# Optimization experiments

Measured on AMD Instinct MI355X. Metric: run time of the kernel, lower is better.

Reference implementation:

```python
import jax, jax.numpy as jnp
import numpy as np

C = 256
EPS = 1e-5
SHIFTS = [(1, 0), (2, 0), (3, 0), (-1, 0), (-2, 0), (-3, 0),
          (0, -1), (0, -2), (0, -3), (0, 1), (0, 2), (0, 3)]
# exp(-(i^2+j^2) / (2 * 1.5^2)) per the module
_WEIGHTS = np.exp(-np.array([i * i + j * j for i, j in SHIFTS], dtype=np.float32)
                  / (2.0 * 1.5 ** 2))
_WSUM = float(_WEIGHTS.sum())


def setup_inputs() -> dict:
    key = jax.random.key(0)
    ks = jax.random.split(key, 12)
    B, H, W = 8, 64, 160
    inp = {
        "x": jax.random.normal(ks[0], (B, C, H, W), dtype=jnp.float32),
        # 1x1 conv: weight [C_out, C_in], bias [C]
        "conv_w": jax.random.normal(ks[1], (C, C), dtype=jnp.float32) * (1.0 / np.sqrt(C)),
        "conv_b": jax.random.normal(ks[2], (C,), dtype=jnp.float32) * 0.01,
        # BatchNorm (eval mode): gamma, beta, running mean/var
        "bn_gamma": jnp.ones((C,), jnp.float32) + 0.1 * jax.random.normal(ks[3], (C,)),
        "bn_beta": 0.1 * jax.random.normal(ks[4], (C,)),
        "bn_mean": 0.1 * jax.random.normal(ks[5], (C,)),
        "bn_var": jnp.abs(jax.random.normal(ks[6], (C,))) + 0.5,
        # depthwise 3x3 conv: weight [C, 1, 3, 3], bias [C]
        "refine_w": jax.random.normal(ks[7], (C, 1, 3, 3), dtype=jnp.float32) * (1.0 / 3.0),
        "refine_b": jax.random.normal(ks[8], (C,), dtype=jnp.float32) * 0.01,
        "rbn_gamma": jnp.ones((C,), jnp.float32) + 0.1 * jax.random.normal(ks[9], (C,)),
        "rbn_beta": 0.1 * jax.random.normal(ks[10], (C,)),
        "rbn_mean": 0.1 * jax.random.normal(ks[11], (C,)),
        "rbn_var": jnp.abs(jax.random.normal(jax.random.fold_in(key, 99), (C,))) + 0.5,
    }
    return inp


def _bn(x, gamma, beta, mean, var):
    # eval-mode BatchNorm2d over NCHW, per-channel stats
    scale = (gamma / jnp.sqrt(var + EPS))[None, :, None, None]
    shift = (beta - mean * gamma / jnp.sqrt(var + EPS))[None, :, None, None]
    return x * scale + shift


def _dwconv3x3(x, w, b):
    # depthwise 3x3, SAME padding, groups = C
    y = jax.lax.conv_general_dilated(
        x, w, window_strides=(1, 1), padding="SAME",
        dimension_numbers=("NCHW", "OIHW", "NCHW"), feature_group_count=C)
    return y + b[None, :, None, None]


def reference(x, conv_w, conv_b, bn_gamma, bn_beta, bn_mean, bn_var,
              refine_w, refine_b, rbn_gamma, rbn_beta, rbn_mean, rbn_var):
    # 1x1 conv + BN + ReLU commutes with spatial roll, so compute it once.
    y = jnp.einsum("bchw,oc->bohw", x, conv_w) + conv_b[None, :, None, None]
    y = jax.nn.relu(_bn(y, bn_gamma, bn_beta, bn_mean, bn_var))

    acc = jnp.zeros_like(x)
    for (sh, sw), wt in zip(SHIFTS, _WEIGHTS):
        ys = jnp.roll(y, shift=(sh, sw), axis=(2, 3))
        contrib = jax.nn.relu(_bn(_dwconv3x3(ys, refine_w, refine_b),
                                  rbn_gamma, rbn_beta, rbn_mean, rbn_var))
        acc = acc + float(wt) * contrib
    return x + 0.5 * acc / _WSUM
```

## Files before the change

### kernel.cpp

```cpp
#include <hip/hip_runtime.h>
#include <hip/hip_bf16.h>

#define EPS 1e-5f

__device__ __forceinline__ unsigned short f2bf(float f) {
    unsigned int u = __builtin_bit_cast(unsigned int, f);
    unsigned int r = u + 0x7FFFu + ((u >> 16) & 1u);
    return (unsigned short)(r >> 16);
}
__device__ __forceinline__ float bf2f(unsigned short b) {
    unsigned int u = ((unsigned int)b) << 16;
    return __builtin_bit_cast(float, u);
}

typedef __attribute__((ext_vector_type(8))) short short8;
typedef __attribute__((ext_vector_type(4))) float floatx4;

#define BM 128
#define BN 128
#define BK 32
#define SK 40

__global__ __launch_bounds__(256) void conv1x1_bn_relu(
    const float* __restrict__ x,
    const float* __restrict__ w,
    const float* __restrict__ cb,
    const float* __restrict__ gamma, const float* __restrict__ beta,
    const float* __restrict__ mean,  const float* __restrict__ var,
    unsigned short* __restrict__ y)
{
    const int nt  = blockIdx.x >> 1;
    const int mb  = blockIdx.x & 1;
    const int b   = blockIdx.z;
    const int tid = threadIdx.x;

    __shared__ unsigned short Al[BM * SK];
    __shared__ unsigned short Bl[BN * SK];
    __shared__ float s1[BM], u1[BM];

    const int m0 = mb * BM;
    const int p0 = nt * BN;

    if (tid < BM) {
        int o = m0 + tid;
        float s = gamma[o] * rsqrtf(var[o] + EPS);
        s1[tid] = s;
        u1[tid] = cb[o] * s + beta[o] - mean[o] * s;
    }

    const float* xb = x + (size_t)b * 256 * 10240;

    floatx4 acc[4][4];
#pragma unroll
    for (int i = 0; i < 4; i++)
#pragma unroll
        for (int j = 0; j < 4; j++) acc[i][j] = (floatx4)0.0f;

    const int lane = tid & 63;
    const int wv   = tid >> 6;
    const int wm   = (wv & 1) * 64;
    const int wn   = (wv >> 1) * 64;
    const int lm   = lane & 15;
    const int lq   = lane >> 4;

    const int nB = tid & 127;
    const int kB = (tid >> 7) * 4;

    for (int k0 = 0; k0 < 256; k0 += BK) {
        __syncthreads();
        {
            int id = tid;
#pragma unroll
            for (int it = 0; it < 4; it++, id += 256) {
                int m  = id >> 3;
                int f4 = id & 7;
                float4 v = *reinterpret_cast<const float4*>(
                    w + (size_t)(m0 + m) * 256 + k0 + f4 * 4);
                *reinterpret_cast<ushort4*>(&Al[m * SK + f4 * 4]) =
                    make_ushort4(f2bf(v.x), f2bf(v.y), f2bf(v.z), f2bf(v.w));
            }
        }
        {
            int kb = kB;
#pragma unroll
            for (int it = 0; it < 4; it++, kb += 8) {
                float v0 = xb[(size_t)(k0 + kb + 0) * 10240 + p0 + nB];
                float v1 = xb[(size_t)(k0 + kb + 1) * 10240 + p0 + nB];
                float v2 = xb[(size_t)(k0 + kb + 2) * 10240 + p0 + nB];
                float v3 = xb[(size_t)(k0 + kb + 3) * 10240 + p0 + nB];
                *reinterpret_cast<ushort4*>(&Bl[nB * SK + kb]) =
                    make_ushort4(f2bf(v0), f2bf(v1), f2bf(v2), f2bf(v3));
            }
        }
        __syncthreads();

        short8 af[4], bfr[4];
#pragma unroll
        for (int i = 0; i < 4; i++) {
            int m = wm + i * 16 + lm;
            af[i] = *reinterpret_cast<const short8*>(&Al[m * SK + lq * 8]);
        }
#pragma unroll
        for (int j = 0; j < 4; j++) {
            int n = wn + j * 16 + lm;
            bfr[j] = *reinterpret_cast<const short8*>(&Bl[n * SK + lq * 8]);
        }
#pragma unroll
        for (int i = 0; i < 4; i++)
#pragma unroll
            for (int j = 0; j < 4; j++)
                acc[i][j] = __builtin_amdgcn_mfma_f32_16x16x32_bf16(
                    af[i], bfr[j], acc[i][j], 0, 0, 0);
    }

    unsigned short* yb = y + (size_t)b * 256 * 10240;
#pragma unroll
    for (int i = 0; i < 4; i++) {
        int mo_base = wm + i * 16 + lq * 4;
#pragma unroll
        for (int j = 0; j < 4; j++) {
            int p = p0 + wn + j * 16 + lm;
#pragma unroll
            for (int r = 0; r < 4; r++) {
                int mo = mo_base + r;
                float v = acc[i][j][r] * s1[mo] + u1[mo];
                v = fmaxf(v, 0.0f);
                yb[(size_t)(m0 + mo) * 10240 + p] = f2bf(v);
            }
        }
    }
}

#define YS 52
#define QS 52

__global__ __launch_bounds__(256) void refine_accum(
    const float* __restrict__ x,
    const unsigned short* __restrict__ y,
    const float* __restrict__ rw,
    const float* __restrict__ rb,
    const float* __restrict__ rg, const float* __restrict__ rbe,
    const float* __restrict__ rm, const float* __restrict__ rv,
    float* __restrict__ out)
{
    const int bi    = blockIdx.x;
    const int strip = bi & 3;
    const int c     = (bi >> 2) & 255;
    const int b     = bi >> 10;
    const int c0    = strip * 40;
    const int tid   = threadIdx.x;

    __shared__ float yt[64 * YS];
    __shared__ float qt[64 * QS];

    const size_t img = ((size_t)b * 256 + c) * 10240;
    const unsigned short* yp = y + img;

    float w9[9];
#pragma unroll
    for (int t = 0; t < 9; t++) w9[t] = rw[c * 9 + t];
    const float s2 = rg[c] * rsqrtf(rv[c] + EPS);
    const float u2 = rb[c] * s2 + rbe[c] - rm[c] * s2;

    for (int id = tid; id < 64 * 50; id += 256) {
        int r = id / 50, j = id - r * 50;
        int gw = c0 - 5 + j;
        if (gw < 0) gw += 160; else if (gw >= 160) gw -= 160;
        yt[r * YS + j] = bf2f(yp[r * 160 + gw]);
    }
    __syncthreads();

    for (int t = tid; t < 64 * 12; t += 256) {
        int r = t / 12, g = t - r * 12;
        int q0 = 4 * g;
        int rm1 = (r + 63) & 63, rp1 = (r + 1) & 63;
        float A[8], B[8], C[8];
        *reinterpret_cast<float4*>(&A[0]) = *reinterpret_cast<const float4*>(&yt[rm1 * YS + q0]);
        *reinterpret_cast<float4*>(&A[4]) = *reinterpret_cast<const float4*>(&yt[rm1 * YS + q0 + 4]);
        *reinterpret_cast<float4*>(&B[0]) = *reinterpret_cast<const float4*>(&yt[r   * YS + q0]);
        *reinterpret_cast<float4*>(&B[4]) = *reinterpret_cast<const float4*>(&yt[r   * YS + q0 + 4]);
        *reinterpret_cast<float4*>(&C[0]) = *reinterpret_cast<const float4*>(&yt[rp1 * YS + q0]);
        *reinterpret_cast<float4*>(&C[4]) = *reinterpret_cast<const float4*>(&yt[rp1 * YS + q0 + 4]);
        float4 qv;
        float* qvp = reinterpret_cast<float*>(&qv);
#pragma unroll
        for (int i = 0; i < 4; i++) {
            float z = w9[0] * A[i] + w9[1] * A[i + 1] + w9[2] * A[i + 2]
                    + w9[3] * B[i] + w9[4] * B[i + 1] + w9[5] * B[i + 2]
                    + w9[6] * C[i] + w9[7] * C[i + 1] + w9[8] * C[i + 2];
            qvp[i] = fmaxf(z * s2 + u2, 0.0f);
        }
        *reinterpret_cast<float4*>(&qt[r * QS + q0]) = qv;
    }
    __syncthreads();

    const float w1 = 0.80073740f, w2 = 0.41111229f, w3 = 0.13533528f;
    const float SCALE = 0.5f / (4.0f * (w1 + w2 + w3));

    for (int t = tid; t < 64 * 10; t += 256) {
        int r = t / 10, g = t - r * 10;
        int qb = 4 * g + 4;
        float vm1[4], vm2[4], vm3[4], vp1[4], vp2[4], vp3[4], H[12];
        *reinterpret_cast<float4*>(&vm1[0]) = *reinterpret_cast<const float4*>(&qt[((r + 63) & 63) * QS + qb]);
        *reinterpret_cast<float4*>(&vm2[0]) = *reinterpret_cast<const float4*>(&qt[((r + 62) & 63) * QS + qb]);
        *reinterpret_cast<float4*>(&vm3[0]) = *reinterpret_cast<const float4*>(&qt[((r + 61) & 63) * QS + qb]);
        *reinterpret_cast<float4*>(&vp1[0]) = *reinterpret_cast<const float4*>(&qt[((r + 1) & 63) * QS + qb]);
        *reinterpret_cast<float4*>(&vp2[0]) = *reinterpret_cast<const float4*>(&qt[((r + 2) & 63) * QS + qb]);
        *reinterpret_cast<float4*>(&vp3[0]) = *reinterpret_cast<const float4*>(&qt[((r + 3) & 63) * QS + qb]);
        *reinterpret_cast<float4*>(&H[0])  = *reinterpret_cast<const float4*>(&qt[r * QS + qb - 4]);
        *reinterpret_cast<float4*>(&H[4])  = *reinterpret_cast<const float4*>(&qt[r * QS + qb]);
        *reinterpret_cast<float4*>(&H[8])  = *reinterpret_cast<const float4*>(&qt[r * QS + qb + 4]);

        int h = r, w0 = c0 + 4 * g;
        size_t gidx = img + (size_t)h * 160 + w0;
        float4 xv = *reinterpret_cast<const float4*>(&x[gidx]);
        const float* xvp = reinterpret_cast<const float*>(&xv);
        float ov[4];
#pragma unroll
        for (int i = 0; i < 4; i++) {
            float vs = w1 * (vm1[i] + vp1[i]) + w2 * (vm2[i] + vp2[i]) + w3 * (vm3[i] + vp3[i]);
            float hs = w1 * (H[i + 3] + H[i + 5]) + w2 * (H[i + 2] + H[i + 6]) + w3 * (H[i + 1] + H[i + 7]);
            ov[i] = xvp[i] + SCALE * (vs + hs);
        }
        bool rowok = (h != 0) && (h != 63);
        if (rowok) {
            if (c0 == 0 && g == 0) {
                out[gidx + 1] = ov[1]; out[gidx + 2] = ov[2]; out[gidx + 3] = ov[3];
            } else if (c0 == 120 && g == 9) {
                out[gidx] = ov[0]; out[gidx + 1] = ov[1]; out[gidx + 2] = ov[2];
            } else {
                *reinterpret_cast<float4*>(&out[gidx]) =
                    make_float4(ov[0], ov[1], ov[2], ov[3]);
            }
        }
    }

    const int SH[12] = {1, 2, 3, -1, -2, -3, 0, 0, 0, 0, 0, 0};
    const int SW[12] = {0, 0, 0, 0, 0, 0, -1, -2, -3, 1, 2, 3};
    const float WT[12] = {w1, w2, w3, w1, w2, w3, w1, w2, w3, w1, w2, w3};
    const bool edge = (c0 == 0) || (c0 == 120);
    const int nb = 80 + (edge ? 62 : 0);
    if (tid < nb) {
        int h, w;
        if (tid < 40)      { h = 0;  w = c0 + tid; }
        else if (tid < 80) { h = 63; w = c0 + tid - 40; }
        else               { h = tid - 79; w = (c0 == 0) ? 0 : 159; }
        float mw[9];
#pragma unroll
        for (int dh = 0; dh < 3; dh++)
#pragma unroll
            for (int dw = 0; dw < 3; dw++) {
                int ih = h + dh - 1, iw = w + dw - 1;
                mw[dh * 3 + dw] =
                    (ih >= 0 && ih < 64 && iw >= 0 && iw < 160) ? w9[dh * 3 + dw] : 0.0f;
            }
        float accv = 0.0f;
#pragma unroll
        for (int s = 0; s < 12; s++) {
            float conv = 0.0f;
#pragma unroll
            for (int dh = 0; dh < 3; dh++)
#pragma unroll
                for (int dw = 0; dw < 3; dw++) {
                    int row = (h + dh - 1 - SH[s]) & 63;
                    int jj  = (w - c0) + dw + 4 - SW[s];
                    conv += mw[dh * 3 + dw] * yt[row * YS + jj];
                }
            accv += WT[s] * fmaxf(conv * s2 + u2, 0.0f);
        }
        size_t gidx = img + (size_t)h * 160 + w;
        out[gidx] = x[gidx] + SCALE * accv;
    }
}

extern "C" void kernel_launch(void* const* d_in, const int* in_sizes, int n_in,
                              void* d_out, int out_size, void* d_ws, size_t ws_size,
                              hipStream_t stream) {
    const float* x      = (const float*)d_in[0];
    const float* conv_w = (const float*)d_in[1];
    const float* conv_b = (const float*)d_in[2];
    const float* bn_g   = (const float*)d_in[3];
    const float* bn_b   = (const float*)d_in[4];
    const float* bn_m   = (const float*)d_in[5];
    const float* bn_v   = (const float*)d_in[6];
    const float* ref_w  = (const float*)d_in[7];
    const float* ref_b  = (const float*)d_in[8];
    const float* rbn_g  = (const float*)d_in[9];
    const float* rbn_b  = (const float*)d_in[10];
    const float* rbn_m  = (const float*)d_in[11];
    const float* rbn_v  = (const float*)d_in[12];
    float* out          = (float*)d_out;
    unsigned short* y_ws = (unsigned short*)d_ws;

    conv1x1_bn_relu<<<dim3(160, 1, 8), 256, 0, stream>>>(
        x, conv_w, conv_b, bn_g, bn_b, bn_m, bn_v, y_ws);
    refine_accum<<<dim3(8 * 256 * 4), 256, 0, stream>>>(
        x, y_ws, ref_w, ref_b, rbn_g, rbn_b, rbn_m, rbn_v, out);
}
```

Baseline: 254.3 us.

## Prefetch GEMM tiles into registers and register-block the refinement stencil stages

The 1x1-conv GEMM now loads the next K-slice of weights and activations into registers while MFMAs run on the current slice. Activations are read as float4 and packed into pairs of bf16, replacing scalar strided loads. In the refinement kernel, each thread copies a contiguous run of the y tile, computes two output rows of the depthwise conv for more row reuse, and handles four rows in the shift-sum stage. The border threads now run alongside the interior threads instead of afterwards. These changes raise register pressure and add some divergence between the two thread groups.

```diff
diff --git a/kernel.cpp b/kernel.cpp
--- a/kernel.cpp
+++ b/kernel.cpp
@@ -11,6 +11,9 @@
 __device__ __forceinline__ float bf2f(unsigned short b) {
     unsigned int u = ((unsigned int)b) << 16;
     return __builtin_bit_cast(float, u);
+}
+__device__ __forceinline__ unsigned int pack2bf(float lo, float hi) {
+    return (unsigned int)f2bf(lo) | ((unsigned int)f2bf(hi) << 16);
 }
 
 typedef __attribute__((ext_vector_type(8))) short short8;
@@ -63,36 +66,56 @@
     const int lm   = lane & 15;
     const int lq   = lane >> 4;
 
-    const int nB = tid & 127;
-    const int kB = (tid >> 7) * 4;
+    const int kk2 = (tid & 15) * 2;
+    const int pg0 = tid >> 4;
+    const int am0 = tid >> 3;
+    const int af4 = tid & 7;
+
+    float4 Ar[4], Br[4];
+
+    auto loadA = [&](int k0) {
+#pragma unroll
+        for (int it = 0; it < 4; it++) {
+            int m = am0 + it * 32;
+            Ar[it] = *reinterpret_cast<const float4*>(
+                w + (size_t)(m0 + m) * 256 + k0 + af4 * 4);
+        }
+    };
+    auto loadB = [&](int k0) {
+        const float* base = xb + (size_t)(k0 + kk2) * 10240 + p0;
+        Br[0] = *reinterpret_cast<const float4*>(base + 4 * pg0);
+        Br[1] = *reinterpret_cast<const float4*>(base + 10240 + 4 * pg0);
+        Br[2] = *reinterpret_cast<const float4*>(base + 4 * (pg0 + 16));
+        Br[3] = *reinterpret_cast<const float4*>(base + 10240 + 4 * (pg0 + 16));
+    };
+
+    loadA(0);
+    loadB(0);
 
     for (int k0 = 0; k0 < 256; k0 += BK) {
         __syncthreads();
+#pragma unroll
+        for (int it = 0; it < 4; it++) {
+            int m = am0 + it * 32;
+            *reinterpret_cast<ushort4*>(&Al[m * SK + af4 * 4]) =
+                make_ushort4(f2bf(Ar[it].x), f2bf(Ar[it].y),
+                             f2bf(Ar[it].z), f2bf(Ar[it].w));
+        }
         {
-            int id = tid;
-#pragma unroll
-            for (int it = 0; it < 4; it++, id += 256) {
-                int m  = id >> 3;
-                int f4 = id & 7;
-                float4 v = *reinterpret_cast<const float4*>(
-                    w + (size_t)(m0 + m) * 256 + k0 + f4 * 4);
-                *reinterpret_cast<ushort4*>(&Al[m * SK + f4 * 4]) =
-                    make_ushort4(f2bf(v.x), f2bf(v.y), f2bf(v.z), f2bf(v.w));
-            }
-        }
-        {
-            int kb = kB;
-#pragma unroll
-            for (int it = 0; it < 4; it++, kb += 8) {
-                float v0 = xb[(size_t)(k0 + kb + 0) * 10240 + p0 + nB];
-                float v1 = xb[(size_t)(k0 + kb + 1) * 10240 + p0 + nB];
-                float v2 = xb[(size_t)(k0 + kb + 2) * 10240 + p0 + nB];
-                float v3 = xb[(size_t)(k0 + kb + 3) * 10240 + p0 + nB];
-                *reinterpret_cast<ushort4*>(&Bl[nB * SK + kb]) =
-                    make_ushort4(f2bf(v0), f2bf(v1), f2bf(v2), f2bf(v3));
+            const float* r0 = reinterpret_cast<const float*>(&Br[0]);
+            const float* r1 = reinterpret_cast<const float*>(&Br[1]);
+            const float* r2 = reinterpret_cast<const float*>(&Br[2]);
+            const float* r3 = reinterpret_cast<const float*>(&Br[3]);
+#pragma unroll
+            for (int i = 0; i < 4; i++) {
+                *reinterpret_cast<unsigned int*>(&Bl[(4 * pg0 + i) * SK + kk2]) =
+                    pack2bf(r0[i], r1[i]);
+                *reinterpret_cast<unsigned int*>(&Bl[(4 * (pg0 + 16) + i) * SK + kk2]) =
+                    pack2bf(r2[i], r3[i]);
             }
         }
         __syncthreads();
+        if (k0 + BK < 256) { loadA(k0 + BK); loadB(k0 + BK); }
 
         short8 af[4], bfr[4];
 #pragma unroll
@@ -162,114 +185,157 @@
     const float s2 = rg[c] * rsqrtf(rv[c] + EPS);
     const float u2 = rb[c] * s2 + rbe[c] - rm[c] * s2;
 
-    for (int id = tid; id < 64 * 50; id += 256) {
-        int r = id / 50, j = id - r * 50;
-        int gw = c0 - 5 + j;
-        if (gw < 0) gw += 160; else if (gw >= 160) gw -= 160;
-        yt[r * YS + j] = bf2f(yp[r * 160 + gw]);
+    {
+        const int r  = tid >> 2;
+        const int j0 = (tid & 3) * 13;
+        const unsigned short* yrow = yp + r * 160;
+        float* drow = &yt[r * YS + j0];
+        const bool mayWrap = (c0 == 0) || (c0 == 120);
+        if (!mayWrap) {
+            const unsigned short* s = yrow + (c0 - 5 + j0);
+#pragma unroll
+            for (int i = 0; i < 13; i++) drow[i] = bf2f(s[i]);
+        } else {
+#pragma unroll
+            for (int i = 0; i < 13; i++) {
+                int gw = c0 - 5 + j0 + i;
+                if (gw < 0) gw += 160; else if (gw >= 160) gw -= 160;
+                drow[i] = bf2f(yrow[gw]);
+            }
+        }
     }
     __syncthreads();
 
-    for (int t = tid; t < 64 * 12; t += 256) {
-        int r = t / 12, g = t - r * 12;
-        int q0 = 4 * g;
-        int rm1 = (r + 63) & 63, rp1 = (r + 1) & 63;
-        float A[8], B[8], C[8];
-        *reinterpret_cast<float4*>(&A[0]) = *reinterpret_cast<const float4*>(&yt[rm1 * YS + q0]);
-        *reinterpret_cast<float4*>(&A[4]) = *reinterpret_cast<const float4*>(&yt[rm1 * YS + q0 + 4]);
-        *reinterpret_cast<float4*>(&B[0]) = *reinterpret_cast<const float4*>(&yt[r   * YS + q0]);
-        *reinterpret_cast<float4*>(&B[4]) = *reinterpret_cast<const float4*>(&yt[r   * YS + q0 + 4]);
-        *reinterpret_cast<float4*>(&C[0]) = *reinterpret_cast<const float4*>(&yt[rp1 * YS + q0]);
-        *reinterpret_cast<float4*>(&C[4]) = *reinterpret_cast<const float4*>(&yt[rp1 * YS + q0 + 4]);
-        float4 qv;
-        float* qvp = reinterpret_cast<float*>(&qv);
+    for (int t = tid; t < 32 * 12; t += 256) {
+        int rbk = t / 12, g = t - rbk * 12;
+        int r0 = 2 * rbk, q0 = 4 * g;
+        int ra = (r0 + 63) & 63, rd = (r0 + 2) & 63;
+        float A[8], B[8], C[8], D[8];
+        *reinterpret_cast<float4*>(&A[0]) = *reinterpret_cast<const float4*>(&yt[ra * YS + q0]);
+        *reinterpret_cast<float4*>(&A[4]) = *reinterpret_cast<const float4*>(&yt[ra * YS + q0 + 4]);
+        *reinterpret_cast<float4*>(&B[0]) = *reinterpret_cast<const float4*>(&yt[r0 * YS + q0]);
+        *reinterpret_cast<float4*>(&B[4]) = *reinterpret_cast<const float4*>(&yt[r0 * YS + q0 + 4]);
+        *reinterpret_cast<float4*>(&C[0]) = *reinterpret_cast<const float4*>(&yt[(r0 + 1) * YS + q0]);
+        *reinterpret_cast<float4*>(&C[4]) = *reinterpret_cast<const float4*>(&yt[(r0 + 1) * YS + q0 + 4]);
+        *reinterpret_cast<float4*>(&D[0]) = *reinterpret_cast<const float4*>(&yt[rd * YS + q0]);
+        *reinterpret_cast<float4*>(&D[4]) = *reinterpret_cast<const float4*>(&yt[rd * YS + q0 + 4]);
+        float4 qlo, qhi;
+        float* ql = reinterpret_cast<float*>(&qlo);
+        float* qh = reinterpret_cast<float*>(&qhi);
 #pragma unroll
         for (int i = 0; i < 4; i++) {
-            float z = w9[0] * A[i] + w9[1] * A[i + 1] + w9[2] * A[i + 2]
-                    + w9[3] * B[i] + w9[4] * B[i + 1] + w9[5] * B[i + 2]
-                    + w9[6] * C[i] + w9[7] * C[i + 1] + w9[8] * C[i + 2];
-            qvp[i] = fmaxf(z * s2 + u2, 0.0f);
-        }
-        *reinterpret_cast<float4*>(&qt[r * QS + q0]) = qv;
+            float z0 = w9[0] * A[i] + w9[1] * A[i + 1] + w9[2] * A[i + 2]
+                     + w9[3] * B[i] + w9[4] * B[i + 1] + w9[5] * B[i + 2]
+                     + w9[6] * C[i] + w9[7] * C[i + 1] + w9[8] * C[i + 2];
+            float z1 = w9[0] * B[i] + w9[1] * B[i + 1] + w9[2] * B[i + 2]
+                     + w9[3] * C[i] + w9[4] * C[i + 1] + w9[5] * C[i + 2]
+                     + w9[6] * D[i] + w9[7] * D[i + 1] + w9[8] * D[i + 2];
+            ql[i] = fmaxf(z0 * s2 + u2, 0.0f);
+            qh[i] = fmaxf(z1 * s2 + u2, 0.0f);
+        }
+        *reinterpret_cast<float4*>(&qt[r0 * QS + q0]) = qlo;
+        *reinterpret_cast<float4*>(&qt[(r0 + 1) * QS + q0]) = qhi;
     }
     __syncthreads();
 
     const float w1 = 0.80073740f, w2 = 0.41111229f, w3 = 0.13533528f;
     const float SCALE = 0.5f / (4.0f * (w1 + w2 + w3));
 
-    for (int t = tid; t < 64 * 10; t += 256) {
-        int r = t / 10, g = t - r * 10;
-        int qb = 4 * g + 4;
-        float vm1[4], vm2[4], vm3[4], vp1[4], vp2[4], vp3[4], H[12];
-        *reinterpret_cast<float4*>(&vm1[0]) = *reinterpret_cast<const float4*>(&qt[((r + 63) & 63) * QS + qb]);
-        *reinterpret_cast<float4*>(&vm2[0]) = *reinterpret_cast<const float4*>(&qt[((r + 62) & 63) * QS + qb]);
-        *reinterpret_cast<float4*>(&vm3[0]) = *reinterpret_cast<const float4*>(&qt[((r + 61) & 63) * QS + qb]);
-        *reinterpret_cast<float4*>(&vp1[0]) = *reinterpret_cast<const float4*>(&qt[((r + 1) & 63) * QS + qb]);
-        *reinterpret_cast<float4*>(&vp2[0]) = *reinterpret_cast<const float4*>(&qt[((r + 2) & 63) * QS + qb]);
-        *reinterpret_cast<float4*>(&vp3[0]) = *reinterpret_cast<const float4*>(&qt[((r + 3) & 63) * QS + qb]);
-        *reinterpret_cast<float4*>(&H[0])  = *reinterpret_cast<const float4*>(&qt[r * QS + qb - 4]);
-        *reinterpret_cast<float4*>(&H[4])  = *reinterpret_cast<const float4*>(&qt[r * QS + qb]);
-        *reinterpret_cast<float4*>(&H[8])  = *reinterpret_cast<const float4*>(&qt[r * QS + qb + 4]);
-
-        int h = r, w0 = c0 + 4 * g;
-        size_t gidx = img + (size_t)h * 160 + w0;
-        float4 xv = *reinterpret_cast<const float4*>(&x[gidx]);
-        const float* xvp = reinterpret_cast<const float*>(&xv);
-        float ov[4];
+    if (tid < 160) {
+        const int rg4 = tid / 10, cg = tid - rg4 * 10;
+        const int r0 = 4 * rg4;
+        const int qb = 4 * cg + 4;
+        const int w0 = c0 + 4 * cg;
+
+        float V[10][4], L[4][4], R[4][4];
+#pragma unroll
+        for (int k = 0; k < 10; k++)
+            *reinterpret_cast<float4*>(&V[k][0]) =
+                *reinterpret_cast<const float4*>(&qt[((r0 - 3 + k + 64) & 63) * QS + qb]);
 #pragma unroll
         for (int i = 0; i < 4; i++) {
-            float vs = w1 * (vm1[i] + vp1[i]) + w2 * (vm2[i] + vp2[i]) + w3 * (vm3[i] + vp3[i]);
-            float hs = w1 * (H[i + 3] + H[i + 5]) + w2 * (H[i + 2] + H[i + 6]) + w3 * (H[i + 1] + H[i + 7]);
-            ov[i] = xvp[i] + SCALE * (vs + hs);
-        }
-        bool rowok = (h != 0) && (h != 63);
-        if (rowok) {
-            if (c0 == 0 && g == 0) {
-                out[gidx + 1] = ov[1]; out[gidx + 2] = ov[2]; out[gidx + 3] = ov[3];
-            } else if (c0 == 120 && g == 9) {
-                out[gidx] = ov[0]; out[gidx + 1] = ov[1]; out[gidx + 2] = ov[2];
-            } else {
-                *reinterpret_cast<float4*>(&out[gidx]) =
-                    make_float4(ov[0], ov[1], ov[2], ov[3]);
-            }
-        }
-    }
-
-    const int SH[12] = {1, 2, 3, -1, -2, -3, 0, 0, 0, 0, 0, 0};
-    const int SW[12] = {0, 0, 0, 0, 0, 0, -1, -2, -3, 1, 2, 3};
-    const float WT[12] = {w1, w2, w3, w1, w2, w3, w1, w2, w3, w1, w2, w3};
-    const bool edge = (c0 == 0) || (c0 == 120);
-    const int nb = 80 + (edge ? 62 : 0);
-    if (tid < nb) {
-        int h, w;
-        if (tid < 40)      { h = 0;  w = c0 + tid; }
-        else if (tid < 80) { h = 63; w = c0 + tid - 40; }
-        else               { h = tid - 79; w = (c0 == 0) ? 0 : 159; }
-        float mw[9];
-#pragma unroll
-        for (int dh = 0; dh < 3; dh++)
-#pragma unroll
-            for (int dw = 0; dw < 3; dw++) {
-                int ih = h + dh - 1, iw = w + dw - 1;
-                mw[dh * 3 + dw] =
-                    (ih >= 0 && ih < 64 && iw >= 0 && iw < 160) ? w9[dh * 3 + dw] : 0.0f;
-            }
-        float accv = 0.0f;
-#pragma unroll
-        for (int s = 0; s < 12; s++) {
-            float conv = 0.0f;
-#pragma unroll
-            for (int dh = 0; dh < 3; dh++)
-#pragma unroll
-                for (int dw = 0; dw < 3; dw++) {
-                    int row = (h + dh - 1 - SH[s]) & 63;
-                    int jj  = (w - c0) + dw + 4 - SW[s];
-                    conv += mw[dh * 3 + dw] * yt[row * YS + jj];
+            *reinterpret_cast<float4*>(&L[i][0]) =
+                *reinterpret_cast<const float4*>(&qt[(r0 + i) * QS + qb - 4]);
+            *reinterpret_cast<float4*>(&R[i][0]) =
+                *reinterpret_cast<const float4*>(&qt[(r0 + i) * QS + qb + 4]);
+        }
+#pragma unroll
+        for (int i = 0; i < 4; i++) {
+            int r = r0 + i;
+            size_t gidx = img + (size_t)r * 160 + w0;
+            float4 xv = *reinterpret_cast<const float4*>(&x[gidx]);
+            const float* xvp = reinterpret_cast<const float*>(&xv);
+            float H[12];
+#pragma unroll
+            for (int j = 0; j < 4; j++) H[j]     = L[i][j];
+#pragma unroll
+            for (int j = 0; j < 4; j++) H[4 + j] = V[i + 3][j];
+#pragma unroll
+            for (int j = 0; j < 4; j++) H[8 + j] = R[i][j];
+            float ov[4];
+#pragma unroll
+            for (int j = 0; j < 4; j++) {
+                float vs = w1 * (V[i + 2][j] + V[i + 4][j])
+                         + w2 * (V[i + 1][j] + V[i + 5][j])
+                         + w3 * (V[i][j]     + V[i + 6][j]);
+                float hs = w1 * (H[3 + j] + H[5 + j])
+                         + w2 * (H[2 + j] + H[6 + j])
+                         + w3 * (H[1 + j] + H[7 + j]);
+                ov[j] = xvp[j] + SCALE * (vs + hs);
+            }
+            bool rowok = (r != 0) && (r != 63);
+            if (rowok) {
+                if (c0 == 0 && cg == 0) {
+                    out[gidx + 1] = ov[1]; out[gidx + 2] = ov[2]; out[gidx + 3] = ov[3];
+                } else if (c0 == 120 && cg == 9) {
+                    out[gidx] = ov[0]; out[gidx + 1] = ov[1]; out[gidx + 2] = ov[2];
+                } else {
+                    *reinterpret_cast<float4*>(&out[gidx]) =
+                        make_float4(ov[0], ov[1], ov[2], ov[3]);
                 }
-            accv += WT[s] * fmaxf(conv * s2 + u2, 0.0f);
-        }
-        size_t gidx = img + (size_t)h * 160 + w;
-        out[gidx] = x[gidx] + SCALE * accv;
+            }
+        }
+    } else {
+        const int SH[12] = {1, 2, 3, -1, -2, -3, 0, 0, 0, 0, 0, 0};
+        const int SW[12] = {0, 0, 0, 0, 0, 0, -1, -2, -3, 1, 2, 3};
+        const float WT[12] = {w1, w2, w3, w1, w2, w3, w1, w2, w3, w1, w2, w3};
+        const bool edge = (c0 == 0) || (c0 == 120);
+        const int nb = 80 + (edge ? 62 : 0);
+#pragma unroll
+        for (int it = 0; it < 2; it++) {
+            int bidx = (tid - 160) + it * 96;
+            if (bidx < nb) {
+                int h, w;
+                if (bidx < 40)      { h = 0;  w = c0 + bidx; }
+                else if (bidx < 80) { h = 63; w = c0 + bidx - 40; }
+                else                { h = bidx - 79; w = (c0 == 0) ? 0 : 159; }
+                float mw[9];
+#pragma unroll
+                for (int dh = 0; dh < 3; dh++)
+#pragma unroll
+                    for (int dw = 0; dw < 3; dw++) {
+                        int ih = h + dh - 1, iw = w + dw - 1;
+                        mw[dh * 3 + dw] =
+                            (ih >= 0 && ih < 64 && iw >= 0 && iw < 160) ? w9[dh * 3 + dw] : 0.0f;
+                    }
+                float accv = 0.0f;
+#pragma unroll
+                for (int s = 0; s < 12; s++) {
+                    float conv = 0.0f;
+#pragma unroll
+                    for (int dh = 0; dh < 3; dh++)
+#pragma unroll
+                        for (int dw = 0; dw < 3; dw++) {
+                            int row = (h + dh - 1 - SH[s]) & 63;
+                            int jj  = (w - c0) + dw + 4 - SW[s];
+                            conv += mw[dh * 3 + dw] * yt[row * YS + jj];
+                        }
+                    accv += WT[s] * fmaxf(conv * s2 + u2, 0.0f);
+                }
+                size_t gidx = img + (size_t)h * 160 + w;
+                out[gidx] = x[gidx] + SCALE * accv;
+            }
+        }
     }
 }
 
```

Measured after the change: 270.9 us. 1.07x slower.

## Pre-cast and transpose GEMM operands to bf16, load via global_load_lds

Applied to the files above, without the earlier changes.

Adds a weight cast kernel and an x transpose-to-bf16 kernel so the 1x1 conv GEMM can stream contiguous bf16 tiles straight into LDS with direct global-to-LDS loads, removing the strided per-element fp32 gathers and in-loop conversion. The refine kernel's halo load also gets a wrap-free fast path for interior strips. This costs two extra launches and an extra full read of x plus a write and re-read of its bf16 copy. The LDS tiles also lose their padding, which may cause bank conflicts, and the path only runs when the workspace is large enough.

```diff
diff --git a/kernel.cpp b/kernel.cpp
--- a/kernel.cpp
+++ b/kernel.cpp
@@ -16,12 +16,155 @@
 typedef __attribute__((ext_vector_type(8))) short short8;
 typedef __attribute__((ext_vector_type(4))) float floatx4;
 
-#define BM 128
-#define BN 128
-#define BK 32
+__device__ __forceinline__ void gload16(const void* g, void* l) {
+    __builtin_amdgcn_global_load_lds(
+        (const __attribute__((address_space(1))) unsigned int*)g,
+        (__attribute__((address_space(3))) unsigned int*)l,
+        16, 0, 0);
+}
+
+__global__ __launch_bounds__(256) void cast_w_kernel(
+    const float* __restrict__ w, unsigned short* __restrict__ wb)
+{
+    int idx = (blockIdx.x * 256 + threadIdx.x) * 4;
+    float4 v = *reinterpret_cast<const float4*>(w + idx);
+    *reinterpret_cast<ushort4*>(wb + idx) =
+        make_ushort4(f2bf(v.x), f2bf(v.y), f2bf(v.z), f2bf(v.w));
+}
+
+#define TS 72
+
+__global__ __launch_bounds__(256) void transpose_x_kernel(
+    const float* __restrict__ x, unsigned short* __restrict__ xT)
+{
+    const int pt = blockIdx.x;
+    const int ct = blockIdx.y;
+    const int b  = blockIdx.z;
+    const int tid = threadIdx.x;
+
+    __shared__ unsigned short T[64 * TS];
+
+    const int p0 = pt * 64, c0 = ct * 64;
+    const float* xb = x + ((size_t)b * 256 + c0) * 10240 + p0;
+
+    {
+        const int cc  = tid >> 2;
+        const int pb  = (tid & 3) * 16;
+        const float* src = xb + (size_t)cc * 10240 + pb;
+#pragma unroll
+        for (int it = 0; it < 4; it++) {
+            float4 v = *reinterpret_cast<const float4*>(src + it * 4);
+            T[(pb + it * 4 + 0) * TS + cc] = f2bf(v.x);
+            T[(pb + it * 4 + 1) * TS + cc] = f2bf(v.y);
+            T[(pb + it * 4 + 2) * TS + cc] = f2bf(v.z);
+            T[(pb + it * 4 + 3) * TS + cc] = f2bf(v.w);
+        }
+    }
+    __syncthreads();
+
+    unsigned short* dst = xT + ((size_t)b * 10240 + p0) * 256 + c0;
+#pragma unroll
+    for (int it = 0; it < 2; it++) {
+        int slot = tid + it * 256;
+        int pp = slot >> 3, sg = slot & 7;
+        *reinterpret_cast<uint4*>(dst + (size_t)pp * 256 + sg * 8) =
+            *reinterpret_cast<const uint4*>(&T[pp * TS + sg * 8]);
+    }
+}
+
+__global__ __launch_bounds__(256) void conv1x1_gemm_async(
+    const unsigned short* __restrict__ xT,
+    const unsigned short* __restrict__ Wb,
+    const float* __restrict__ cb,
+    const float* __restrict__ gamma, const float* __restrict__ beta,
+    const float* __restrict__ mean,  const float* __restrict__ var,
+    unsigned short* __restrict__ y)
+{
+    const int nt  = blockIdx.x >> 1;
+    const int mb  = blockIdx.x & 1;
+    const int b   = blockIdx.z;
+    const int tid = threadIdx.x;
+
+    __shared__ unsigned short Al[128 * 32];
+    __shared__ unsigned short Bl[128 * 32];
+    __shared__ float s1[128], u1[128];
+
+    const int m0 = mb * 128;
+    const int p0 = nt * 128;
+
+    if (tid < 128) {
+        int o = m0 + tid;
+        float s = gamma[o] * rsqrtf(var[o] + EPS);
+        s1[tid] = s;
+        u1[tid] = cb[o] * s + beta[o] - mean[o] * s;
+    }
+
+    const int lane = tid & 63;
+    const int wv   = tid >> 6;
+    const int lm   = lane & 15;
+    const int lq   = lane >> 4;
+    const int wm   = (wv & 1) * 64;
+    const int wn   = (wv >> 1) * 64;
+
+    const int srow = wv * 32 + (lane >> 2);
+    const int kg   = (lane & 3) * 8;
+    const unsigned short* gA = Wb + (size_t)(m0 + srow) * 256 + kg;
+    const unsigned short* gB = xT + ((size_t)b * 10240 + p0 + srow) * 256 + kg;
+    unsigned short* lA0 = &Al[(wv * 32) * 32];
+    unsigned short* lA1 = &Al[(wv * 32 + 16) * 32];
+    unsigned short* lB0 = &Bl[(wv * 32) * 32];
+    unsigned short* lB1 = &Bl[(wv * 32 + 16) * 32];
+
+    floatx4 acc[4][4];
+#pragma unroll
+    for (int i = 0; i < 4; i++)
+#pragma unroll
+        for (int j = 0; j < 4; j++) acc[i][j] = (floatx4)0.0f;
+
+#pragma unroll
+    for (int k0 = 0; k0 < 256; k0 += 32) {
+        __syncthreads();
+        gload16(gA + k0, lA0);
+        gload16(gA + 16 * 256 + k0, lA1);
+        gload16(gB + k0, lB0);
+        gload16(gB + 16 * 256 + k0, lB1);
+        __syncthreads();
+
+        short8 af[4], bfr[4];
+#pragma unroll
+        for (int i = 0; i < 4; i++)
+            af[i] = *reinterpret_cast<const short8*>(&Al[(wm + i * 16 + lm) * 32 + lq * 8]);
+#pragma unroll
+        for (int j = 0; j < 4; j++)
+            bfr[j] = *reinterpret_cast<const short8*>(&Bl[(wn + j * 16 + lm) * 32 + lq * 8]);
+#pragma unroll
+        for (int i = 0; i < 4; i++)
+#pragma unroll
+            for (int j = 0; j < 4; j++)
+                acc[i][j] = __builtin_amdgcn_mfma_f32_16x16x32_bf16(
+                    af[i], bfr[j], acc[i][j], 0, 0, 0);
+    }
+
+    unsigned short* yb = y + (size_t)b * 256 * 10240;
+#pragma unroll
+    for (int i = 0; i < 4; i++) {
+        int mo_base = wm + i * 16 + lq * 4;
+#pragma unroll
+        for (int j = 0; j < 4; j++) {
+            int p = p0 + wn + j * 16 + lm;
+#pragma unroll
+            for (int r = 0; r < 4; r++) {
+                int mo = mo_base + r;
+                float v = acc[i][j][r] * s1[mo] + u1[mo];
+                v = fmaxf(v, 0.0f);
+                yb[(size_t)(m0 + mo) * 10240 + p] = f2bf(v);
+            }
+        }
+    }
+}
+
 #define SK 40
-
-__global__ __launch_bounds__(256) void conv1x1_bn_relu(
+__global__ __launch_bounds__(256) void conv1x1_bn_relu_fb(
     const float* __restrict__ x,
     const float* __restrict__ w,
     const float* __restrict__ cb,
@@ -34,20 +177,19 @@
     const int b   = blockIdx.z;
     const int tid = threadIdx.x;
 
-    __shared__ unsigned short Al[BM * SK];
-    __shared__ unsigned short Bl[BN * SK];
-    __shared__ float s1[BM], u1[BM];
-
-    const int m0 = mb * BM;
-    const int p0 = nt * BN;
-
-    if (tid < BM) {
+    __shared__ unsigned short Al[128 * SK];
+    __shared__ unsigned short Bl[128 * SK];
+    __shared__ float s1[128], u1[128];
+
+    const int m0 = mb * 128;
+    const int p0 = nt * 128;
+
+    if (tid < 128) {
         int o = m0 + tid;
         float s = gamma[o] * rsqrtf(var[o] + EPS);
         s1[tid] = s;
         u1[tid] = cb[o] * s + beta[o] - mean[o] * s;
     }
-
     const float* xb = x + (size_t)b * 256 * 10240;
 
     floatx4 acc[4][4];
@@ -62,18 +204,16 @@
     const int wn   = (wv >> 1) * 64;
     const int lm   = lane & 15;
     const int lq   = lane >> 4;
-
     const int nB = tid & 127;
     const int kB = (tid >> 7) * 4;
 
-    for (int k0 = 0; k0 < 256; k0 += BK) {
+    for (int k0 = 0; k0 < 256; k0 += 32) {
         __syncthreads();
         {
             int id = tid;
 #pragma unroll
             for (int it = 0; it < 4; it++, id += 256) {
-                int m  = id >> 3;
-                int f4 = id & 7;
+                int m = id >> 3, f4 = id & 7;
                 float4 v = *reinterpret_cast<const float4*>(
                     w + (size_t)(m0 + m) * 256 + k0 + f4 * 4);
                 *reinterpret_cast<ushort4*>(&Al[m * SK + f4 * 4]) =
@@ -93,18 +233,13 @@
             }
         }
         __syncthreads();
-
         short8 af[4], bfr[4];
 #pragma unroll
-        for (int i = 0; i < 4; i++) {
-            int m = wm + i * 16 + lm;
-            af[i] = *reinterpret_cast<const short8*>(&Al[m * SK + lq * 8]);
-        }
-#pragma unroll
-        for (int j = 0; j < 4; j++) {
-            int n = wn + j * 16 + lm;
-            bfr[j] = *reinterpret_cast<const short8*>(&Bl[n * SK + lq * 8]);
-        }
+        for (int i = 0; i < 4; i++)
+            af[i] = *reinterpret_cast<const short8*>(&Al[(wm + i * 16 + lm) * SK + lq * 8]);
+#pragma unroll
+        for (int j = 0; j < 4; j++)
+            bfr[j] = *reinterpret_cast<const short8*>(&Bl[(wn + j * 16 + lm) * SK + lq * 8]);
 #pragma unroll
         for (int i = 0; i < 4; i++)
 #pragma unroll
@@ -112,7 +247,6 @@
                 acc[i][j] = __builtin_amdgcn_mfma_f32_16x16x32_bf16(
                     af[i], bfr[j], acc[i][j], 0, 0, 0);
     }
-
     unsigned short* yb = y + (size_t)b * 256 * 10240;
 #pragma unroll
     for (int i = 0; i < 4; i++) {
@@ -124,8 +258,7 @@
             for (int r = 0; r < 4; r++) {
                 int mo = mo_base + r;
                 float v = acc[i][j][r] * s1[mo] + u1[mo];
-                v = fmaxf(v, 0.0f);
-                yb[(size_t)(m0 + mo) * 10240 + p] = f2bf(v);
+                yb[(size_t)(m0 + mo) * 10240 + p] = f2bf(fmaxf(v, 0.0f));
             }
         }
     }
@@ -162,11 +295,24 @@
     const float s2 = rg[c] * rsqrtf(rv[c] + EPS);
     const float u2 = rb[c] * s2 + rbe[c] - rm[c] * s2;
 
-    for (int id = tid; id < 64 * 50; id += 256) {
-        int r = id / 50, j = id - r * 50;
-        int gw = c0 - 5 + j;
-        if (gw < 0) gw += 160; else if (gw >= 160) gw -= 160;
-        yt[r * YS + j] = bf2f(yp[r * 160 + gw]);
+    {
+        const int r  = tid >> 2;
+        const int j0 = (tid & 3) * 13;
+        const unsigned short* yrow = yp + r * 160;
+        float* drow = &yt[r * YS + j0];
+        const bool mayWrap = (c0 == 0) || (c0 == 120);
+        if (!mayWrap) {
+            const unsigned short* s = yrow + (c0 - 5 + j0);
+#pragma unroll
+            for (int i = 0; i < 13; i++) drow[i] = bf2f(s[i]);
+        } else {
+#pragma unroll
+            for (int i = 0; i < 13; i++) {
+                int gw = c0 - 5 + j0 + i;
+                if (gw < 0) gw += 160; else if (gw >= 160) gw -= 160;
+                drow[i] = bf2f(yrow[gw]);
+            }
+        }
     }
     __syncthreads();
 
@@ -290,10 +436,25 @@
     const float* rbn_m  = (const float*)d_in[11];
     const float* rbn_v  = (const float*)d_in[12];
     float* out          = (float*)d_out;
+
+    const size_t Y_BYTES  = (size_t)8 * 256 * 10240 * 2;
+    const size_t XT_BYTES = Y_BYTES;
+    const size_t W_BYTES  = 256 * 256 * 2;
+
     unsigned short* y_ws = (unsigned short*)d_ws;
 
-    conv1x1_bn_relu<<<dim3(160, 1, 8), 256, 0, stream>>>(
-        x, conv_w, conv_b, bn_g, bn_b, bn_m, bn_v, y_ws);
+    if (ws_size >= Y_BYTES + XT_BYTES + W_BYTES) {
+        unsigned short* xT = (unsigned short*)((char*)d_ws + Y_BYTES);
+        unsigned short* Wb = (unsigned short*)((char*)d_ws + Y_BYTES + XT_BYTES);
+        cast_w_kernel<<<dim3(64), 256, 0, stream>>>(conv_w, Wb);
+        transpose_x_kernel<<<dim3(160, 4, 8), 256, 0, stream>>>(x, xT);
+        conv1x1_gemm_async<<<dim3(160, 1, 8), 256, 0, stream>>>(
+            xT, Wb, conv_b, bn_g, bn_b, bn_m, bn_v, y_ws);
+    } else {
+        conv1x1_bn_relu_fb<<<dim3(160, 1, 8), 256, 0, stream>>>(
+            x, conv_w, conv_b, bn_g, bn_b, bn_m, bn_v, y_ws);
+    }
+
     refine_accum<<<dim3(8 * 256 * 4), 256, 0, stream>>>(
         x, y_ws, ref_w, ref_b, rbn_g, rbn_b, rbn_m, rbn_v, out);
 }
```

Result: slower. 275.7 us (+8.4%).
